# Performance work log

Measured on AMD Instinct MI355X. Metric: run time of the kernel, lower is better.

Reference implementation:

```python
import jax, jax.numpy as jnp
import numpy as np

D = 1024
B = 16
SP = 256
T = B * SP
DT_REF = 1.0
MAX_GROWTH = 0.3


def _cayley(re, im):
    A = re + 1j * im
    A = A - A.conj().T  # skew-Hermitian part
    I = jnp.eye(A.shape[0], dtype=A.dtype)
    return jnp.linalg.solve(I + A, I - A)


def _dft_basis(d):
    n = jnp.arange(d)
    k = jnp.arange(d)[:, None]
    ang = -2.0 * jnp.pi * (k * n).astype(jnp.float32) / d
    return jnp.exp(1j * ang) / jnp.sqrt(jnp.float32(d))


def _forward(x_input, h_prev_re, h_prev_im, xg_re, xg_im, flux_re, flux_im, dt,
             u_raw_re, u_raw_im, v_raw_re, v_raw_im, log_sigma, dft_weight,
             decay_re, decay_im, Wi, bi, Wo, bo, Wg, bg,
             ld, lf, law_re, law_im, base_noise, Wu1, bu1, Wu2, bu2,
             noise_re, noise_im):
    d = x_input.shape[-1]
    # ---- basis.encode ----
    V = _cayley(v_raw_re, v_raw_im)                       # [D,D] complex
    s_diag = jnp.exp(log_sigma).astype(V.dtype)
    xc = x_input.astype(jnp.complex64)
    alpha = jax.nn.sigmoid(dft_weight)
    x_tilde = (xc @ V) * s_diag * (1.0 - alpha) + (xc @ _dft_basis(d)) * alpha
    x_tilde = x_tilde[:, None, :]                          # [T,1,D]
    # ---- flux_tracker.forward_step ----
    fdecay = jax.nn.sigmoid(decay_re) + 1j * decay_im
    x_cat = jnp.concatenate([xg_re, xg_im], axis=-1)       # [B,2D]
    xin = x_cat @ Wi.T + bi
    update = xin[..., :d] + 1j * xin[..., d:]
    flux_next = (flux_re + 1j * flux_im) * fdecay + update
    s_cat = jnp.concatenate([flux_next.real, flux_next.imag], axis=-1)
    proj = s_cat @ Wo.T + bo
    source = proj[..., :d] + 1j * proj[..., d:]            # [B,D] complex
    gate = jax.nn.sigmoid(s_cat @ Wg.T + bg)               # [B,D] real
    # ---- transition operators ----
    l_re = jnp.tanh(-jnp.exp(ld) + law_re) * MAX_GROWTH
    lam = l_re + 1j * (lf + law_im)
    dt_ratio = dt / DT_REF                                 # [1]
    op_decay = jnp.exp(lam[None, :] * dt_ratio[:, None].astype(jnp.complex64))
    op_forcing = (op_decay - 1.0) / (lam[None, :] + 1e-8)
    # ---- expand source/gate over spatial ----
    bsz = source.shape[0]
    sp = x_tilde.shape[0] // bsz
    src = jnp.broadcast_to(source[:, None, None, :], (bsz, sp, 1, d)).reshape(-1, 1, d)
    g = jnp.broadcast_to(gate[:, None, None, :], (bsz, sp, 1, d)).reshape(-1, 1, d)
    forcing = x_tilde * g + src * (1.0 - g)
    h_prev = h_prev_re + 1j * h_prev_im
    h_next = h_prev * op_decay + forcing * op_forcing      # [T,1,D]
    # ---- SDE stochastic term ----
    base_var = base_noise ** 2 * jnp.expm1(2.0 * l_re * dt_ratio[:, None]) / (2.0 * l_re + 1e-8)
    base_var = jnp.maximum(base_var, 0.0)                  # [1,D]
    h_mean = h_next.mean(axis=1).real                      # [T,D]
    u = jax.nn.softplus(jax.nn.silu(h_mean @ Wu1.T + bu1) @ Wu2.T + bu2)  # [T,D]
    std = jnp.sqrt(base_var * u)[:, None, :].astype(h_next.dtype)          # [T,1,D]
    noise = (noise_re + 1j * noise_im) * jnp.sqrt(jnp.float32(0.5))
    return h_next + noise * std, flux_next


def setup_inputs() -> dict:
    key = jax.random.key(0)
    ks = jax.random.split(key, 40)
    rn = lambda i, shp, sc=1.0: jax.random.normal(ks[i], shp, jnp.float32) * sc
    q_re = jnp.linalg.qr(rn(0, (D, D)))[0]
    q_im = jnp.linalg.qr(rn(1, (D, D)))[0]
    return {
        "x_input": rn(2, (T, D)),
        "h_prev_re": rn(3, (T, 1, D)), "h_prev_im": rn(4, (T, 1, D)),
        "xg_re": rn(5, (B, D)), "xg_im": rn(6, (B, D)),
        "flux_re": rn(7, (B, D)), "flux_im": rn(8, (B, D)),
        "dt": jnp.ones((1,), jnp.float32),
        "u_raw_re": q_re * 0.1, "u_raw_im": q_im * 0.1,
        "v_raw_re": q_re.T * 0.1, "v_raw_im": q_im.T * 0.1,
        "log_sigma": jnp.zeros((D,), jnp.float32),
        "dft_weight": jnp.float32(0.2),
        "decay_re": rn(9, (D,), 0.1) - 1.0, "decay_im": rn(10, (D,), 0.1),
        "Wi": rn(11, (2 * D, 2 * D), 0.02), "bi": jnp.zeros((2 * D,), jnp.float32),
        "Wo": rn(12, (2 * D, 2 * D), 0.02), "bo": jnp.zeros((2 * D,), jnp.float32),
        "Wg": rn(13, (D, 2 * D), 0.02), "bg": jnp.zeros((D,), jnp.float32),
        "ld": rn(14, (D,), 0.5) - 2.0, "lf": rn(15, (D,), 1.0),
        "law_re": rn(16, (D,), 0.01), "law_im": rn(17, (D,), 0.01),
        "base_noise": jnp.float32(0.01),
        "Wu1": rn(18, (D // 4, D), 0.03), "bu1": jnp.zeros((D // 4,), jnp.float32),
        "Wu2": rn(19, (D, D // 4), 0.06), "bu2": jnp.zeros((D,), jnp.float32),
        "noise_re": rn(20, (T, 1, D)), "noise_im": rn(21, (T, 1, D)),
    }


def reference(x_input, h_prev_re, h_prev_im, xg_re, xg_im, flux_re, flux_im, dt,
              u_raw_re, u_raw_im, v_raw_re, v_raw_im, log_sigma, dft_weight,
              decay_re, decay_im, Wi, bi, Wo, bo, Wg, bg,
              ld, lf, law_re, law_im, base_noise, Wu1, bu1, Wu2, bu2,
              noise_re, noise_im):
    return _forward(x_input, h_prev_re, h_prev_im, xg_re, xg_im, flux_re, flux_im, dt,
                    u_raw_re, u_raw_im, v_raw_re, v_raw_im, log_sigma, dft_weight,
                    decay_re, decay_im, Wi, bi, Wo, bo, Wg, bg,
                    ld, lf, law_re, law_im, base_noise, Wu1, bu1, Wu2, bu2,
                    noise_re, noise_im)
```

## Files before the change

### kernel.cpp

```cpp
#include <hip/hip_runtime.h>
#include <cstddef>

#define TPB 256
#define TPB2 512

typedef short bf8v  __attribute__((ext_vector_type(8)));
typedef float f32x4 __attribute__((ext_vector_type(4)));
typedef unsigned short u16;

#define PSZ 2048
#define PSZ2 4096
#define LSTR 40
#define BUF1 2560
#define CSTR 68

static __device__ __forceinline__ u16 f2bf(float x) {
  unsigned int u = __float_as_uint(x);
  u = (u + 0x7FFFu + ((u >> 16) & 1u)) >> 16;
  return (u16)u;
}
static __device__ __forceinline__ float bf2f(u16 x) {
  return __uint_as_float(((unsigned int)x) << 16);
}
static __device__ __forceinline__ float sigmoidf_(float x) {
  return 1.0f / (1.0f + __expf(-x));
}
static __device__ __forceinline__ float spf_(float v) {
  return (v > 15.0f) ? v : __logf(1.0f + __expf(v));
}
static __device__ __forceinline__ bf8v neg8(bf8v a) {
  #pragma unroll
  for (int i = 0; i < 8; ++i) a[i] ^= (short)0x8000;
  return a;
}
static __device__ __forceinline__ void pack8(const float4& x, const float4& y,
                                             u16* dst) {
  unsigned int* d = (unsigned int*)dst;
  d[0] = ((unsigned)f2bf(x.y) << 16) | f2bf(x.x);
  d[1] = ((unsigned)f2bf(x.w) << 16) | f2bf(x.z);
  d[2] = ((unsigned)f2bf(y.y) << 16) | f2bf(y.x);
  d[3] = ((unsigned)f2bf(y.w) << 16) | f2bf(y.z);
}
static __device__ __forceinline__ uint2 packbf4(float a, float b, float c, float d) {
  uint2 r;
  r.x = ((unsigned)f2bf(b) << 16) | f2bf(a);
  r.y = ((unsigned)f2bf(d) << 16) | f2bf(c);
  return r;
}
static __device__ __forceinline__ void gload16(const u16* g, u16* l) {
  __builtin_amdgcn_global_load_lds((const __attribute__((address_space(1))) void*)g,
                                   (__attribute__((address_space(3))) void*)l,
                                   16, 0, 0);
}
static __device__ __forceinline__ bf8v fragld(const u16* plane, int r, int kq) {
  int kb = (kq << 4) ^ (((r >> 1) & 3) << 4);
  return *(const bf8v*)(plane + r * 32 + (kb >> 1));
}
static __device__ __forceinline__ bf8v fragld2(const u16* plane, int r, int kq, int s) {
  int ch = ((s << 2) + kq) ^ (r & 7);
  return *(const bf8v*)(plane + r * 64 + (ch << 3));
}
static __device__ __forceinline__ int swz8(int flat, int T) {
  return (flat & 7) * (T >> 3) + (flat >> 3);
}

#define WAITV(n) asm volatile("s_waitcnt vmcnt(" #n ")" ::: "memory")

__global__ __launch_bounds__(TPB) void build_a_k(
    const float* __restrict__ vre, const float* __restrict__ vim,
    u16* __restrict__ Ar, u16* __restrict__ Ai,
    u16* __restrict__ Nr, u16* __restrict__ Ni)
{
  int idx = blockIdx.x * TPB + threadIdx.x;
  int i = idx >> 10, j = idx & 1023;
  float ar = vre[idx] - vre[j * 1024 + i];
  float ai = vim[idx] + vim[j * 1024 + i];
  float dg = (i == j) ? 1.0f : 0.0f;
  Ar[idx] = f2bf(ar);       Ai[idx] = f2bf(ai);
  Nr[idx] = f2bf(dg - ar);  Ni[idx] = f2bf(-ai);
}

#define CG_VARS                                                              \
  int lane = tid & 63;                                                       \
  int wr = (tid >> 7) & 1, wc = (tid >> 6) & 1;                              \
  int lr8_ = ((tid & 63) >> 3) + ((tid >> 6) << 4);                          \
  int ks2_ = (((lane & 7) ^ (lane >> 3)) << 3);                              \
  u16* Lw_ = lds + ((tid >> 6) << 10);                                       \
  f32x4 accR[2][2] = {};                                                     \
  f32x4 accI[2][2] = {};

#define CG_STAGE(buf, k0, PAr, PAi, PBr, PBi)                                \
  { u16* Lb = Lw_ + (buf) * (4 * PSZ2);                                      \
    gload16((PAr) + (size_t)(bm + lr8_) * 1024 + (k0) + ks2_,     Lb + 0 * PSZ2);       \
    gload16((PAr) + (size_t)(bm + lr8_ + 8) * 1024 + (k0) + ks2_, Lb + 0 * PSZ2 + 512); \
    gload16((PAi) + (size_t)(bm + lr8_) * 1024 + (k0) + ks2_,     Lb + 1 * PSZ2);       \
    gload16((PAi) + (size_t)(bm + lr8_ + 8) * 1024 + (k0) + ks2_, Lb + 1 * PSZ2 + 512); \
    gload16((PBr) + (size_t)(bn + lr8_) * 1024 + (k0) + ks2_,     Lb + 2 * PSZ2);       \
    gload16((PBr) + (size_t)(bn + lr8_ + 8) * 1024 + (k0) + ks2_, Lb + 2 * PSZ2 + 512); \
    gload16((PBi) + (size_t)(bn + lr8_) * 1024 + (k0) + ks2_,     Lb + 3 * PSZ2);       \
    gload16((PBi) + (size_t)(bn + lr8_ + 8) * 1024 + (k0) + ks2_, Lb + 3 * PSZ2 + 512); }

#define CG_FRAGS(buf, s)                                                     \
  const u16* L = lds + (buf) * (4 * PSZ2);                                   \
  int rA = wr * 32 + (lane & 15);                                            \
  int rB = wc * 32 + (lane & 15);                                            \
  int kq = lane >> 4;                                                        \
  bf8v ar[2], ai[2], br[2], bi[2];                                           \
  ar[0] = fragld2(L + 0 * PSZ2, rA, kq, s);  ar[1] = fragld2(L + 0 * PSZ2, rA + 16, kq, s); \
  ai[0] = fragld2(L + 1 * PSZ2, rA, kq, s);  ai[1] = fragld2(L + 1 * PSZ2, rA + 16, kq, s); \
  br[0] = fragld2(L + 2 * PSZ2, rB, kq, s);  br[1] = fragld2(L + 2 * PSZ2, rB + 16, kq, s); \
  bi[0] = fragld2(L + 3 * PSZ2, rB, kq, s);  bi[1] = fragld2(L + 3 * PSZ2, rB + 16, kq, s);

#define CG_MFMA_BNEG0                                                        \
  { bf8v nbr[2] = { neg8(br[0]), neg8(br[1]) };                              \
    bf8v nbi[2] = { neg8(bi[0]), neg8(bi[1]) };                              \
    _Pragma("unroll")                                                        \
    for (int mf = 0; mf < 2; ++mf)                                           \
      _Pragma("unroll")                                                      \
      for (int nf = 0; nf < 2; ++nf) {                                       \
        accR[mf][nf] = __builtin_amdgcn_mfma_f32_16x16x32_bf16(ar[mf], nbr[nf], accR[mf][nf], 0, 0, 0); \
        accR[mf][nf] = __builtin_amdgcn_mfma_f32_16x16x32_bf16(ai[mf], nbi[nf], accR[mf][nf], 0, 0, 0); \
        accI[mf][nf] = __builtin_amdgcn_mfma_f32_16x16x32_bf16(ar[mf], bi[nf],  accI[mf][nf], 0, 0, 0); \
        accI[mf][nf] = __builtin_amdgcn_mfma_f32_16x16x32_bf16(ai[mf], nbr[nf], accI[mf][nf], 0, 0, 0); \
      } }

#define CG_MFMA_BNEG1                                                        \
  { bf8v nbi[2] = { neg8(bi[0]), neg8(bi[1]) };                              \
    _Pragma("unroll")                                                        \
    for (int mf = 0; mf < 2; ++mf)                                           \
      _Pragma("unroll")                                                      \
      for (int nf = 0; nf < 2; ++nf) {                                       \
        accR[mf][nf] = __builtin_amdgcn_mfma_f32_16x16x32_bf16(ar[mf], br[nf],  accR[mf][nf], 0, 0, 0); \
        accR[mf][nf] = __builtin_amdgcn_mfma_f32_16x16x32_bf16(ai[mf], bi[nf],  accR[mf][nf], 0, 0, 0); \
        accI[mf][nf] = __builtin_amdgcn_mfma_f32_16x16x32_bf16(ar[mf], nbi[nf], accI[mf][nf], 0, 0, 0); \
        accI[mf][nf] = __builtin_amdgcn_mfma_f32_16x16x32_bf16(ai[mf], br[nf],  accI[mf][nf], 0, 0, 0); \
      } }

#define CG_PIPELINE(MFMA_OP, PAr, PAi, PBr, PBi)                             \
  CG_STAGE(0, 0, PAr, PAi, PBr, PBi);                                        \
  _Pragma("unroll 1")                                                        \
  for (int t = 0; t < 16; ++t) {                                             \
    int bufc = t & 1;                                                        \
    if (t + 1 < 16) { CG_STAGE(bufc ^ 1, (t + 1) * 64, PAr, PAi, PBr, PBi);  \
                      WAITV(8); }                                            \
    else            { WAITV(0); }                                            \
    __builtin_amdgcn_sched_barrier(0);                                       \
    __builtin_amdgcn_s_barrier();                                            \
    __builtin_amdgcn_s_setprio(1);                                           \
    { CG_FRAGS(bufc, 0) MFMA_OP }                                            \
    { CG_FRAGS(bufc, 1) MFMA_OP }                                            \
    __builtin_amdgcn_s_setprio(0);                                           \
    __builtin_amdgcn_sched_barrier(0);                                       \
    __builtin_amdgcn_s_barrier();                                            \
  }

#define CG8_VARS                                                             \
  int lane = tid & 63;                                                       \
  int wv = tid >> 6;                                                         \
  int wq = wv & 3;                                                           \
  int wr = wq >> 1, wc = wq & 1;                                             \
  int sh = wv >> 2;                                                          \
  int ln8 = lane >> 3;                                                       \
  int ks2_ = (((lane & 7) ^ ln8) << 3);                                      \
  f32x4 accR[2][2] = {};                                                     \
  f32x4 accI[2][2] = {};

#define CG8_STAGE(buf, k0, PAr, PAi, PBr, PBi)                               \
  { u16* Lb = lds + (buf) * (4 * PSZ2);                                      \
    _Pragma("unroll")                                                        \
    for (int j = 0; j < 4; ++j) {                                            \
      int idx4 = wv * 4 + j;                                                 \
      int pl = idx4 >> 3, gr = idx4 & 7;                                     \
      const u16* src = (pl == 0) ? (PAr) : (pl == 1) ? (PAi)                 \
                      : (pl == 2) ? (PBr) : (PBi);                           \
      int base = (pl < 2) ? bm : bn;                                         \
      gload16(src + (size_t)(base + gr * 8 + ln8) * 1024 + (k0) + ks2_,      \
              Lb + pl * PSZ2 + gr * 512);                                    \
    } }

#define CG8_PIPELINE(MFMA_OP, PAr, PAi, PBr, PBi)                            \
  CG8_STAGE(0, 0, PAr, PAi, PBr, PBi);                                       \
  _Pragma("unroll 1")                                                        \
  for (int t = 0; t < 16; ++t) {                                             \
    int bufc = t & 1;                                                        \
    if (t + 1 < 16) { CG8_STAGE(bufc ^ 1, (t + 1) * 64, PAr, PAi, PBr, PBi); \
                      WAITV(4); }                                            \
    else            { WAITV(0); }                                            \
    __builtin_amdgcn_sched_barrier(0);                                       \
    __builtin_amdgcn_s_barrier();                                            \
    __builtin_amdgcn_s_setprio(1);                                           \
    { CG_FRAGS(bufc, sh) MFMA_OP }                                           \
    __builtin_amdgcn_s_setprio(0);                                           \
    __builtin_amdgcn_sched_barrier(0);                                       \
    __builtin_amdgcn_s_barrier();                                            \
  }

#define CG8_COMBINE                                                          \
  float* cmb = (float*)lds;                                                  \
  __syncthreads();                                                           \
  if (sh == 1) {                                                             \
    int cb = (wq * 64 + lane) * 33;                                          \
    _Pragma("unroll")                                                        \
    for (int mf = 0; mf < 2; ++mf)                                           \
      _Pragma("unroll")                                                      \
      for (int nf = 0; nf < 2; ++nf)                                         \
        _Pragma("unroll")                                                    \
        for (int r = 0; r < 4; ++r) {                                        \
          cmb[cb + (mf * 2 + nf) * 8 + r]     = accR[mf][nf][r];             \
          cmb[cb + (mf * 2 + nf) * 8 + 4 + r] = accI[mf][nf][r];             \
        }                                                                    \
  }                                                                          \
  __syncthreads();                                                           \
  if (sh == 0) {                                                             \
    int cb = (wq * 64 + lane) * 33;                                          \
    _Pragma("unroll")                                                        \
    for (int mf = 0; mf < 2; ++mf)                                           \
      _Pragma("unroll")                                                      \
      for (int nf = 0; nf < 2; ++nf)                                         \
        _Pragma("unroll")                                                    \
        for (int r = 0; r < 4; ++r) {                                        \
          accR[mf][nf][r] += cmb[cb + (mf * 2 + nf) * 8 + r];                \
          accI[mf][nf][r] += cmb[cb + (mf * 2 + nf) * 8 + 4 + r];            \
        }                                                                    \
  }

__global__ __launch_bounds__(TPB2) void d2_k(
    const u16* __restrict__ Apr, const u16* __restrict__ Api,
    u16* __restrict__ A2r, u16* __restrict__ A2i,
    const float* __restrict__ X, const float* __restrict__ Wu1,
    const float* __restrict__ Wu2,
    const float* __restrict__ ld, const float* __restrict__ lf,
    const float* __restrict__ law_re, const float* __restrict__ law_im,
    const float* __restrict__ dt, const float* __restrict__ base_noise,
    u16* __restrict__ Xb, u16* __restrict__ Wu1b, u16* __restrict__ Wu2b,
    float* __restrict__ od_re, float* __restrict__ od_im,
    float* __restrict__ of_re, float* __restrict__ of_im,
    float* __restrict__ bvar,
    const float* __restrict__ xg_re, const float* __restrict__ xg_im,
    const float* __restrict__ Wi, float* __restrict__ PpI)
{
  __shared__ __align__(16) u16 lds[2 * 4 * PSZ2];
  int tid = threadIdx.x;
  int bx = blockIdx.x;
  if (bx < 256) {
    int flat = swz8(bx, 256);
    int bm = (flat >> 4) * 64, bn = (flat & 15) * 64;
    CG8_VARS
    CG8_PIPELINE(CG_MFMA_BNEG0, Apr, Api, Apr, Api)
    CG8_COMBINE
    if (sh == 0) {
      #pragma unroll
      for (int mf = 0; mf < 2; ++mf)
        #pragma unroll
        for (int nf = 0; nf < 2; ++nf) {
          int col = bn + wc * 32 + nf * 16 + (lane & 15);
          #pragma unroll
          for (int r = 0; r < 4; ++r) {
            int rowg = bm + wr * 32 + mf * 16 + (lane >> 4) * 4 + r;
            size_t o = (size_t)rowg * 1024 + col;
            A2r[o] = f2bf(accR[mf][nf][r]);
            A2i[o] = f2bf(accI[mf][nf][r]);
          }
        }
    }
  } else if (bx < 1408) {
    int e = ((bx - 256) * TPB2 + tid) << 3;
    const float* src;
    u16* dst;
    if (e < 4194304)       { src = X + e;               dst = Xb + e; }
    else if (e < 4456448)  { src = Wu1 + (e - 4194304); dst = Wu1b + (e - 4194304); }
    else                   { src = Wu2 + (e - 4456448); dst = Wu2b + (e - 4456448); }
    float4 a = *(const float4*)src;
    float4 b = *(const float4*)(src + 4);
    u16 tmp[8];
    pack8(a, b, tmp);
    *(bf8v*)dst = *(bf8v*)tmp;
  } else if (bx < 1410) {
    int d = (bx - 1408) * TPB2 + tid;
    float dtr = dt[0];
    float lre = tanhf(-expf(ld[d]) + law_re[d]) * 0.3f;
    float lim = lf[d] + law_im[d];
    float er = expf(lre * dtr);
    float sn, cs;
    sincosf(lim * dtr, &sn, &cs);
    float odr = er * cs, odi = er * sn;
    od_re[d] = odr;  od_im[d] = odi;
    float numr = odr - 1.0f, numi = odi;
    float denr = lre + 1e-8f, deni = lim;
    float inv = 1.0f / (denr * denr + deni * deni);
    of_re[d] = (numr * denr + numi * deni) * inv;
    of_im[d] = (numi * denr - numr * deni) * inv;
    float bn2 = base_noise[0];
    float bv = bn2 * bn2 * expm1f(2.0f * lre * dtr) / (2.0f * lre + 1e-8f);
    bvar[d] = fmaxf(bv, 0.0f);
  } else {
    int id = bx - 1410;
    int c0 = (id & 31) * 64;
    int kbase = (id >> 5) * 256;
    bool act = tid < 256;
    int lane = tid & 63;
    int w = (tid >> 6) & 3;
    int row = (tid & 255) >> 2, kq = (tid & 3) << 3;

    f32x4 acc = {};
    float4 pb0, pb1;
    u16* sl = lds;

    auto gload = [&](int k0) {
      const float* p = Wi + (size_t)(c0 + row) * 2048 + k0 + kq;
      pb0 = *(const float4*)p; pb1 = *(const float4*)(p + 4);
    };
    auto stolds = [&](int buf) {
      pack8(pb0, pb1, sl + buf * BUF1 + row * LSTR + kq);
    };
    auto compute = [&](int buf, int k0) {
      int ar = lane & 15;
      int ko = (lane >> 4) * 8;
      const float* ap = (k0 < 1024) ? (xg_re + (size_t)ar * 1024 + k0 + ko)
                                    : (xg_im + (size_t)ar * 1024 + k0 + ko - 1024);
      float4 a0 = *(const float4*)ap, a1 = *(const float4*)(ap + 4);
      u16 abuf[8];
      pack8(a0, a1, abuf);
      bf8v af = *(bf8v*)abuf;
      bf8v bfr = *(const bf8v*)(sl + buf * BUF1 + (w * 16 + (lane & 15)) * LSTR + ko);
      acc = __builtin_amdgcn_mfma_f32_16x16x32_bf16(af, bfr, acc, 0, 0, 0);
    };

    if (act) { gload(kbase); stolds(0); }
    __syncthreads();
    int cur = 0;
    for (int t = 0; t < 8; ++t) {
      int k0 = kbase + t * 32;
      if (act) {
        if (t < 7) gload(k0 + 32);
        compute(cur, k0);
        if (t < 7) stolds(cur ^ 1);
      }
      __syncthreads();
      cur ^= 1;
    }
    if (act) {
      int c = c0 + w * 16 + (lane & 15);
      #pragma unroll
      for (int r = 0; r < 4; ++r) {
        int rr = (lane >> 4) * 4 + r;
        PpI[((size_t)(id >> 5) * 16 + rr) * 2048 + c] = acc[r];
      }
    }
  }
}

__global__ __launch_bounds__(TPB) void d3_k(
    const u16* __restrict__ A2r, const u16* __restrict__ A2i,
    const u16* __restrict__ Nr2, const u16* __restrict__ Ni2,
    u16* __restrict__ A4r, u16* __restrict__ A4i,
    u16* __restrict__ T1r, u16* __restrict__ T1i,
    const float* __restrict__ PpI, const float* __restrict__ bi,
    float* __restrict__ xin)
{
  __shared__ __align__(16) u16 lds[2 * 4 * PSZ2];
  int tid = threadIdx.x;
  int bx = blockIdx.x;
  if (bx < 512) {
    int flat = swz8(bx, 512);
    int z = flat >> 8;
    int t8 = flat & 255;
    int bm = (t8 >> 4) * 64, bn = (t8 & 15) * 64;
    const u16* Apr = z ? Nr2 : A2r;
    const u16* Api = z ? Ni2 : A2i;
    u16* Cr16 = z ? T1r : A4r;
    u16* Ci16 = z ? T1i : A4i;
    CG_VARS
    CG_PIPELINE(CG_MFMA_BNEG1, Apr, Api, A2r, A2i)
    #pragma unroll
    for (int mf = 0; mf < 2; ++mf)
      #pragma unroll
      for (int nf = 0; nf < 2; ++nf) {
        int col = bn + wc * 32 + nf * 16 + (lane & 15);
        #pragma unroll
        for (int r = 0; r < 4; ++r) {
          int rowg = bm + wr * 32 + mf * 16 + (lane >> 4) * 4 + r;
          size_t o = (size_t)rowg * 1024 + col;
          float vr = accR[mf][nf][r], vi = accI[mf][nf][r];
          if (z) { vr += bf2f(Nr2[o]); vi += bf2f(Ni2[o]); }
          Cr16[o] = f2bf(vr);
          Ci16[o] = f2bf(vi);
        }
      }
  } else {
    int idx = (bx - 512) * TPB + tid;
    int c = idx & 2047;
    float v = bi[c];
    #pragma unroll
    for (int s = 0; s < 8; ++s) v += PpI[(size_t)s * 32768 + idx];
    xin[idx] = v;
  }
}

__global__ __launch_bounds__(TPB2) void d4_k(
    const u16* __restrict__ T1r, const u16* __restrict__ T1i,
    const u16* __restrict__ A4r, const u16* __restrict__ A4i,
    const float* __restrict__ log_sigma, const float* __restrict__ dft_weight,
    u16* __restrict__ Mtr, u16* __restrict__ Mti,
    const float* __restrict__ xin,
    const float* __restrict__ flux_re, const float* __restrict__ flux_im,
    const float* __restrict__ decay_re, const float* __restrict__ decay_im,
    float* __restrict__ FNr, float* __restrict__ FNi,
    float* __restrict__ out1)
{
  __shared__ __align__(16) u16 lds[2 * 4 * PSZ2];
  int tid = threadIdx.x;
  int bx = blockIdx.x;
  if (bx < 256) {
    int flat = swz8(bx, 256);
    int bm = (flat >> 4) * 64, bn = (flat & 15) * 64;
    CG8_VARS
    CG8_PIPELINE(CG_MFMA_BNEG1, T1r, T1i, A4r, A4i)
    CG8_COMBINE

    u16* mtLr = lds;
    u16* mtLi = lds + 4608;
    __syncthreads();
    if (sh == 0) {
      float alpha = sigmoidf_(dft_weight[0]);
      const float isq = 0.03125f * alpha;
      #pragma unroll
      for (int mf = 0; mf < 2; ++mf)
        #pragma unroll
        for (int nf = 0; nf < 2; ++nf) {
          int dl = wc * 32 + nf * 16 + (lane & 15);
          int dgl = bn + dl;
          float w1 = expf(log_sigma[dgl]) * (1.0f - alpha);
          #pragma unroll
          for (int r = 0; r < 4; ++r) {
            int kl = wr * 32 + mf * 16 + (lane >> 4) * 4 + r;
            int kgl = bm + kl;
            size_t o = (size_t)kgl * 1024 + dgl;
            float dg = (kgl == dgl) ? 1.0f : 0.0f;
            float vr = 2.0f * accR[mf][nf][r] + 2.0f * bf2f(T1r[o]) - dg;
            float vi = 2.0f * accI[mf][nf][r] + 2.0f * bf2f(T1i[o]);
            int mm = (kgl * dgl) & 1023;
            float ang = -6.283185307179586f * (float)mm * (1.0f / 1024.0f);
            float sn, cs;
            sincosf(ang, &sn, &cs);
            mtLr[dl * 72 + kl] = f2bf(vr * w1 + cs * isq);
            mtLi[dl * 72 + kl] = f2bf(vi * w1 + sn * isq);
          }
        }
    }
    __syncthreads();
    if (tid < 256) {
      int dl = tid >> 2, kl0 = (tid & 3) * 16;
      size_t o = (size_t)(bn + dl) * 1024 + bm + kl0;
      uint4* srcR = (uint4*)(mtLr + dl * 72 + kl0);
      uint4* srcI = (uint4*)(mtLi + dl * 72 + kl0);
      *(uint4*)(Mtr + o)     = srcR[0];
      *(uint4*)(Mtr + o + 8) = srcR[1];
      *(uint4*)(Mti + o)     = srcI[0];
      *(uint4*)(Mti + o + 8) = srcI[1];
    }
  } else {
    int idx = (bx - 256) * TPB2 + tid;
    int b = idx >> 10, d = idx & 1023;
    float fdr = sigmoidf_(decay_re[d]);
    float fdi = decay_im[d];
    float fr = flux_re[idx], fi = flux_im[idx];
    float ur = xin[b * 2048 + d], ui = xin[b * 2048 + 1024 + d];
    float nr = fr * fdr - fi * fdi + ur;
    float ni = fr * fdi + fi * fdr + ui;
    FNr[idx] = nr;  FNi[idx] = ni;
    out1[idx] = nr;
  }
}

__global__ __launch_bounds__(TPB) void sgemm16_wog_k(
    const float* __restrict__ A0, const float* __restrict__ A1,
    const float* __restrict__ Wo, const float* __restrict__ Wg,
    float* __restrict__ PpO, float* __restrict__ PpG)
{
  __shared__ __align__(16) u16 lds[2 * BUF1];
  int tid = threadIdx.x;
  int bx = blockIdx.x;
  const float* Bw = (bx < 32) ? Wo : Wg;
  float* Pp = (bx < 32) ? PpO : PpG;
  int N = (bx < 32) ? 2048 : 1024;
  int c0 = ((bx < 32) ? bx : (bx - 32)) * 64;
  int kbase = blockIdx.y * 256;
  int lane = tid & 63;
  int w = tid >> 6;
  int row = tid >> 2, kq = (tid & 3) << 3;

  f32x4 acc = {};
  float4 pb0, pb1;

  auto gload = [&](int k0) {
    const float* p = Bw + (size_t)(c0 + row) * 2048 + k0 + kq;
    pb0 = *(const float4*)p; pb1 = *(const float4*)(p + 4);
  };
  auto stolds = [&](int buf) {
    pack8(pb0, pb1, lds + buf * BUF1 + row * LSTR + kq);
  };
  auto compute = [&](int buf, int k0) {
    int ar = lane & 15;
    int ko = (lane >> 4) * 8;
    const float* ap = (k0 < 1024) ? (A0 + (size_t)ar * 1024 + k0 + ko)
                                  : (A1 + (size_t)ar * 1024 + k0 + ko - 1024);
    float4 a0 = *(const float4*)ap, a1 = *(const float4*)(ap + 4);
    u16 abuf[8];
    pack8(a0, a1, abuf);
    bf8v af = *(bf8v*)abuf;
    const u16* L = lds + buf * BUF1;
    bf8v bfr = *(const bf8v*)(L + (w * 16 + (lane & 15)) * LSTR + ko);
    acc = __builtin_amdgcn_mfma_f32_16x16x32_bf16(af, bfr, acc, 0, 0, 0);
  };

  gload(kbase); stolds(0); __syncthreads();
  int cur = 0;
  for (int t = 0; t < 8; ++t) {
    int k0 = kbase + t * 32;
    if (t < 7) gload(k0 + 32);
    compute(cur, k0);
    if (t < 7) stolds(cur ^ 1);
    __syncthreads();
    cur ^= 1;
  }

  int c = c0 + w * 16 + (lane & 15);
  #pragma unroll
  for (int r = 0; r < 4; ++r) {
    int rr = (lane >> 4) * 4 + r;
    Pp[((size_t)blockIdx.y * 16 + rr) * N + c] = acc[r];
  }
}

__global__ __launch_bounds__(TPB) void red16_wog_k(
    const float* __restrict__ PpO, const float* __restrict__ PpG,
    const float* __restrict__ bo, const float* __restrict__ bg,
    float* __restrict__ proj, float* __restrict__ gate)
{
  int idx = blockIdx.x * TPB + threadIdx.x;
  if (idx < 32768) {
    int c = idx & 2047;
    float v = bo[c];
    #pragma unroll
    for (int s = 0; s < 8; ++s) v += PpO[(size_t)s * 32768 + idx];
    proj[idx] = v;
  } else {
    int j = idx - 32768;
    int c = j & 1023;
    float v = bg[c];
    #pragma unroll
    for (int s = 0; s < 8; ++s) v += PpG[(size_t)s * 16384 + j];
    gate[j] = sigmoidf_(v);
  }
}

__global__ __launch_bounds__(TPB) void xmh_nt_k(
    const u16* __restrict__ Xb,
    const u16* __restrict__ Mtr, const u16* __restrict__ Mti,
    const float* __restrict__ gate, const float* __restrict__ proj,
    const float* __restrict__ od_re, const float* __restrict__ od_im,
    const float* __restrict__ of_re, const float* __restrict__ of_im,
    const float* __restrict__ hp_re, const float* __restrict__ hp_im,
    u16* __restrict__ Hrb)
{
  __shared__ __align__(16) u16 lds[2 * 16384];
  int flat = swz8(blockIdx.x, 512);
  int bm = (flat >> 4) * 128, bn = (flat & 15) * 64;
  int tid = threadIdx.x;
  int lane = tid & 63;
  int w = tid >> 6;
  int wr = w >> 1, wc = w & 1;
  int ln8 = lane >> 3;
  int ks2_ = (((lane & 7) ^ ln8) << 3);

  f32x4 accR[4][2] = {};
  f32x4 accI[4][2] = {};

#define XM_STAGE(buf, k0)                                                    \
  { u16* Lb = lds + (buf) * 16384;                                           \
    _Pragma("unroll")                                                        \
    for (int g = 0; g < 4; ++g)                                              \
      gload16(Xb + (size_t)(bm + w * 32 + g * 8 + ln8) * 1024 + (k0) + ks2_, \
              Lb + (w * 32 + g * 8) * 64);                                   \
    _Pragma("unroll")                                                        \
    for (int g = 0; g < 2; ++g) {                                            \
      gload16(Mtr + (size_t)(bn + w * 16 + g * 8 + ln8) * 1024 + (k0) + ks2_,\
              Lb + 8192 + (w * 16 + g * 8) * 64);                            \
      gload16(Mti + (size_t)(bn + w * 16 + g * 8 + ln8) * 1024 + (k0) + ks2_,\
              Lb + 12288 + (w * 16 + g * 8) * 64);                           \
    } }
#define XM_COMPUTE(buf, s)                                                   \
  { const u16* L = lds + (buf) * 16384;                                      \
    int kq = lane >> 4;                                                      \
    bf8v a[4], br[2], bi[2];                                                 \
    _Pragma("unroll")                                                        \
    for (int mf = 0; mf < 4; ++mf)                                           \
      a[mf] = fragld2(L, wr * 64 + mf * 16 + (lane & 15), kq, s);            \
    _Pragma("unroll")                                                        \
    for (int nf = 0; nf < 2; ++nf) {                                         \
      br[nf] = fragld2(L + 8192,  wc * 32 + nf * 16 + (lane & 15), kq, s);   \
      bi[nf] = fragld2(L + 12288, wc * 32 + nf * 16 + (lane & 15), kq, s);   \
    }                                                                        \
    _Pragma("unroll")                                                        \
    for (int mf = 0; mf < 4; ++mf)                                           \
      _Pragma("unroll")                                                      \
      for (int nf = 0; nf < 2; ++nf) {                                       \
        accR[mf][nf] = __builtin_amdgcn_mfma_f32_16x16x32_bf16(a[mf], br[nf], accR[mf][nf], 0, 0, 0); \
        accI[mf][nf] = __builtin_amdgcn_mfma_f32_16x16x32_bf16(a[mf], bi[nf], accI[mf][nf], 0, 0, 0); \
      } }

  XM_STAGE(0, 0);
  #pragma unroll 1
  for (int t = 0; t < 16; ++t) {
    int bufc = t & 1;
    if (t + 1 < 16) { XM_STAGE(bufc ^ 1, (t + 1) * 64); WAITV(8); }
    else            { WAITV(0); }
    __builtin_amdgcn_sched_barrier(0);
    __builtin_amdgcn_s_barrier();
    __builtin_amdgcn_s_setprio(1);
    XM_COMPUTE(bufc, 0)
    XM_COMPUTE(bufc, 1)
    __builtin_amdgcn_s_setprio(0);
    __builtin_amdgcn_sched_barrier(0);
    __builtin_amdgcn_s_barrier();
  }

  #pragma unroll
  for (int mf = 0; mf < 4; ++mf)
    #pragma unroll
    for (int nf = 0; nf < 2; ++nf) {
      int c = bn + wc * 32 + nf * 16 + (lane & 15);
      #pragma unroll
      for (int r = 0; r < 4; ++r) {
        int t = bm + wr * 64 + mf * 16 + (lane >> 4) * 4 + r;
        int b = t >> 8;
        float g  = gate[b * 1024 + c];
        float sr = proj[b * 2048 + c];
        float si = proj[b * 2048 + 1024 + c];
        float fr = accR[mf][nf][r] * g + sr * (1.0f - g);
        float fi = accI[mf][nf][r] * g + si * (1.0f - g);
        float odr = od_re[c], odi = od_im[c];
        float ofr = of_re[c], ofi = of_im[c];
        size_t off = (size_t)t * 1024 + c;
        float pr = hp_re[off], pi = hp_im[off];
        Hrb[off] = f2bf(pr * odr - pi * odi + fr * ofr - fi * ofi);
      }
    }
}

template<int KI, int EPI>
__global__ __launch_bounds__(TPB) void rgemm_nt_k(
    const u16* __restrict__ A, const u16* __restrict__ B,
    const float* __restrict__ bias,
    u16* __restrict__ C16, int nbxl, int total)
{
  __shared__ __align__(16) u16 lds[3 * 2 * PSZ];
  const int K = KI * 32;
  int tid = threadIdx.x;
  int flat = swz8(blockIdx.x, total);
  int bm = (flat >> nbxl) * 64;
  int bn = (flat & ((1 << nbxl) - 1)) * 64;
  const int N = 64 << nbxl;
  int lane = tid & 63;
  int wr = (tid >> 7) & 1, wc = (tid >> 6) & 1;
  int lr_ = ((tid & 63) >> 2) + ((tid >> 6) << 4);
  int ks_ = (((tid & 3) ^ ((tid >> 3) & 3)) << 3);
  u16* Lw_ = lds + ((tid >> 6) << 9);

  f32x4 acc[2][2] = {};

#define RG_STAGE(buf, k0)                                                    \
  { u16* Lb = Lw_ + (buf) * (2 * PSZ);                                       \
    gload16(A + (size_t)(bm + lr_) * K + (k0) + ks_, Lb + 0 * PSZ);          \
    gload16(B + (size_t)(bn + lr_) * K + (k0) + ks_, Lb + 1 * PSZ); }
#define RG_COMPUTE(buf)                                                      \
  { const u16* L = lds + (buf) * (2 * PSZ);                                  \
    int rA = wr * 32 + (lane & 15);                                          \
    int rB = wc * 32 + (lane & 15);                                          \
    int kq = lane >> 4;                                                      \
    bf8v a[2], b[2];                                                         \
    a[0] = fragld(L + 0 * PSZ, rA, kq);  a[1] = fragld(L + 0 * PSZ, rA + 16, kq); \
    b[0] = fragld(L + 1 * PSZ, rB, kq);  b[1] = fragld(L + 1 * PSZ, rB + 16, kq); \
    _Pragma("unroll")                                                        \
    for (int mf = 0; mf < 2; ++mf)                                           \
      _Pragma("unroll")                                                      \
      for (int nf = 0; nf < 2; ++nf)                                         \
        acc[mf][nf] = __builtin_amdgcn_mfma_f32_16x16x32_bf16(a[mf], b[nf], acc[mf][nf], 0, 0, 0); }

  RG_STAGE(0, 0);
  RG_STAGE(1, 32);
  #pragma unroll 1
  for (int t = 0; t < KI; ++t) {
    int bufc = t % 3;
    if (t + 2 < KI) { RG_STAGE((t + 2) % 3, (t + 2) * 32); }
    if (t + 2 < KI)      { WAITV(4); }
    else if (t + 1 < KI) { WAITV(2); }
    else                 { WAITV(0); }
    __builtin_amdgcn_sched_barrier(0);
    __builtin_amdgcn_s_barrier();
    __builtin_amdgcn_s_setprio(1);
    RG_COMPUTE(bufc)
    __builtin_amdgcn_s_setprio(0);
    __builtin_amdgcn_sched_barrier(0);
    __builtin_amdgcn_s_barrier();
  }

  if constexpr (EPI == 0) {
    #pragma unroll
    for (int mf = 0; mf < 2; ++mf)
      #pragma unroll
      for (int nf = 0; nf < 2; ++nf) {
        int c = bn + wc * 32 + nf * 16 + (lane & 15);
        #pragma unroll
        for (int r = 0; r < 4; ++r) {
          int t = bm + wr * 32 + mf * 16 + (lane >> 4) * 4 + r;
          float v = acc[mf][nf][r] + bias[c];
          v = v * sigmoidf_(v);
          C16[(size_t)t * N + c] = f2bf(v);
        }
      }
  } else {
    float* ct = (float*)lds;
    __syncthreads();
    #pragma unroll
    for (int mf = 0; mf < 2; ++mf)
      #pragma unroll
      for (int nf = 0; nf < 2; ++nf) {
        int rbase = wr * 32 + mf * 16 + (lane >> 4) * 4;
        int cc = wc * 32 + nf * 16 + (lane & 15);
        #pragma unroll
        for (int r = 0; r < 4; ++r)
          ct[(rbase + r) * CSTR + cc] = acc[mf][nf][r];
      }
    __syncthreads();
    int w = tid >> 6, l = tid & 63;
    int lcol = (l & 15) * 4;
    #pragma unroll
    for (int p = 0; p < 4; ++p) {
      int lrow = w * 16 + p * 4 + (l >> 4);
      int t = bm + lrow;
      int c = bn + lcol;
      float4 v4 = *(float4*)&ct[lrow * CSTR + lcol];
      float4 bi4 = *(const float4*)(bias + c);
      float u0 = spf_(v4.x + bi4.x);
      float u1 = spf_(v4.y + bi4.y);
      float u2 = spf_(v4.z + bi4.z);
      float u3 = spf_(v4.w + bi4.w);
      *(uint2*)(C16 + (size_t)t * N + c) = packbf4(u0, u1, u2, u3);
    }
  }
}

__global__ __launch_bounds__(TPB) void fin_k(
    const u16* __restrict__ Hrb, const u16* __restrict__ ub,
    const float* __restrict__ nre, const float* __restrict__ bvar,
    float* __restrict__ out0)
{
  int idx = (blockIdx.x * TPB + threadIdx.x) << 3;
  int c = idx & 1023;
  bf8v hb = *(const bf8v*)(Hrb + idx);
  bf8v uv = *(const bf8v*)(ub + idx);
  float4 n0 = *(const float4*)(nre + idx);
  float4 n1 = *(const float4*)(nre + idx + 4);
  float4 b0 = *(const float4*)(bvar + c);
  float4 b1 = *(const float4*)(bvar + c + 4);
  float4 o0, o1;
  const float s2 = 0.7071067811865476f;
  #pragma unroll
  for (int j = 0; j < 4; ++j) {
    float sc = sqrtf(((const float*)&b0)[j] * bf2f((u16)uv[j])) * s2;
    ((float*)&o0)[j] = bf2f((u16)hb[j]) + ((const float*)&n0)[j] * sc;
  }
  #pragma unroll
  for (int j = 0; j < 4; ++j) {
    float sc = sqrtf(((const float*)&b1)[j] * bf2f((u16)uv[4 + j])) * s2;
    ((float*)&o1)[j] = bf2f((u16)hb[4 + j]) + ((const float*)&n1)[j] * sc;
  }
  *(float4*)(out0 + idx)     = o0;
  *(float4*)(out0 + idx + 4) = o1;
}

extern "C" void kernel_launch(void* const* d_in, const int* in_sizes, int n_in,
                              void* d_out, int out_size, void* d_ws, size_t ws_size,
                              hipStream_t stream) {
  (void)in_sizes; (void)n_in; (void)out_size;

  const float* x_input    = (const float*)d_in[0];
  const float* h_prev_re  = (const float*)d_in[1];
  const float* h_prev_im  = (const float*)d_in[2];
  const float* xg_re      = (const float*)d_in[3];
  const float* xg_im      = (const float*)d_in[4];
  const float* flux_re    = (const float*)d_in[5];
  const float* flux_im    = (const float*)d_in[6];
  const float* dt         = (const float*)d_in[7];
  const float* v_raw_re   = (const float*)d_in[10];
  const float* v_raw_im   = (const float*)d_in[11];
  const float* log_sigma  = (const float*)d_in[12];
  const float* dft_weight = (const float*)d_in[13];
  const float* decay_re   = (const float*)d_in[14];
  const float* decay_im   = (const float*)d_in[15];
  const float* Wi_in      = (const float*)d_in[16];
  const float* bi         = (const float*)d_in[17];
  const float* Wo         = (const float*)d_in[18];
  const float* bo         = (const float*)d_in[19];
  const float* Wg         = (const float*)d_in[20];
  const float* bg         = (const float*)d_in[21];
  const float* ld         = (const float*)d_in[22];
  const float* lf         = (const float*)d_in[23];
  const float* law_re     = (const float*)d_in[24];
  const float* law_im     = (const float*)d_in[25];
  const float* base_noise = (const float*)d_in[26];
  const float* Wu1        = (const float*)d_in[27];
  const float* bu1        = (const float*)d_in[28];
  const float* Wu2        = (const float*)d_in[29];
  const float* bu2        = (const float*)d_in[30];
  const float* noise_re   = (const float*)d_in[31];

  const size_t PL16 = 1024ull * 1024ull;
  if (ws_size < 16 * PL16 * 2) return;

  u16* P = (u16*)d_ws;
  u16* Ar  = P + 0 * PL16;   u16* Ai  = P + 1 * PL16;
  u16* Nr  = P + 2 * PL16;   u16* Ni  = P + 3 * PL16;
  u16* A2r = P + 4 * PL16;   u16* A2i = P + 5 * PL16;
  u16* A4r = P + 6 * PL16;   u16* A4i = P + 7 * PL16;
  u16* T1r = P + 8 * PL16;   u16* T1i = P + 9 * PL16;
  u16* Mtr = P + 2 * PL16;   u16* Mti = P + 3 * PL16;
  u16* Xb  = P + 10 * PL16;
  u16* Hrb = P + 4 * PL16;
  u16* ub  = P + 0 * PL16;
  float* PpO = (float*)(P + 0 * PL16);
  float* PpG = PpO + 262144;
  float* PpI = (float*)(P + 14 * PL16);
  u16* mlp1b = P + 14 * PL16;
  u16* Wu1b  = P + 15 * PL16;
  u16* Wu2b  = Wu1b + 262144;
  float* sm  = (float*)(P + 15 * PL16 + 524288);
  float* xin  = sm;
  float* proj = xin + 32768;
  float* FNr  = proj + 32768;
  float* FNi  = FNr + 16384;
  float* gate = FNi + 16384;
  float* od_re = gate + 16384;
  float* od_im = od_re + 1024;
  float* of_re = od_im + 1024;
  float* of_im = of_re + 1024;
  float* bvar  = of_im + 1024;

  float* out0f = (float*)d_out;
  float* out1f = out0f + (size_t)4096 * 1024;

  build_a_k<<<4096, TPB, 0, stream>>>(v_raw_re, v_raw_im, Ar, Ai, Nr, Ni);
  d2_k<<<1666, TPB2, 0, stream>>>(Ar, Ai, A2r, A2i,
                                  x_input, Wu1, Wu2,
                                  ld, lf, law_re, law_im, dt, base_noise,
                                  Xb, Wu1b, Wu2b,
                                  od_re, od_im, of_re, of_im, bvar,
                                  xg_re, xg_im, Wi_in, PpI);
  d3_k<<<640, TPB, 0, stream>>>(A2r, A2i, Nr, Ni, A4r, A4i, T1r, T1i,
                                PpI, bi, xin);
  d4_k<<<288, TPB2, 0, stream>>>(T1r, T1i, A4r, A4i, log_sigma, dft_weight,
                                 Mtr, Mti,
                                 xin, flux_re, flux_im, decay_re, decay_im,
                                 FNr, FNi, out1f);
  sgemm16_wog_k<<<dim3(48, 8), TPB, 0, stream>>>(FNr, FNi, Wo, Wg, PpO, PpG);
  red16_wog_k<<<192, TPB, 0, stream>>>(PpO, PpG, bo, bg, proj, gate);
  xmh_nt_k<<<512, TPB, 0, stream>>>(Xb, Mtr, Mti, gate, proj,
                                    od_re, od_im, of_re, of_im,
                                    h_prev_re, h_prev_im, Hrb);
  rgemm_nt_k<32, 0><<<256, TPB, 0, stream>>>(Hrb, Wu1b, bu1, mlp1b, 2, 256);
  rgemm_nt_k<8, 2><<<1024, TPB, 0, stream>>>(mlp1b, Wu2b, bu2, ub, 4, 1024);
  fin_k<<<2048, TPB, 0, stream>>>(Hrb, ub, noise_re, bvar, out0f);
}
```

Before: 136.4 us.

## Replace split-K 512-thread complex GEMM tiles with 64x32 tiles at 256 threads

The d2 and d4 complex bf16 GEMMs move from 64x64 output tiles, where eight waves split K in half and combine partial sums through LDS, to 64x32 tiles with four waves each covering the full K range. This doubles the block count to 512 and removes the LDS combine step and its extra barriers. The side tasks fused into d2 and d4 (bf16 conversion, operator precompute, small GEMV, flux update) are reindexed for 256-thread blocks. The cost is that A tiles are now loaded by twice as many blocks, raising global and L2 traffic, and each wave does less MFMA work per LDS fragment load.

```diff
diff --git a/kernel.cpp b/kernel.cpp
--- a/kernel.cpp
+++ b/kernel.cpp
@@ -2,7 +2,6 @@
 #include <cstddef>
 
 #define TPB 256
-#define TPB2 512
 
 typedef short bf8v  __attribute__((ext_vector_type(8)));
 typedef float f32x4 __attribute__((ext_vector_type(4)));
@@ -13,6 +12,7 @@
 #define LSTR 40
 #define BUF1 2560
 #define CSTR 68
+#define RTBUF 12288
 
 static __device__ __forceinline__ u16 f2bf(float x) {
   unsigned int u = __float_as_uint(x);
@@ -110,19 +110,6 @@
   ai[0] = fragld2(L + 1 * PSZ2, rA, kq, s);  ai[1] = fragld2(L + 1 * PSZ2, rA + 16, kq, s); \
   br[0] = fragld2(L + 2 * PSZ2, rB, kq, s);  br[1] = fragld2(L + 2 * PSZ2, rB + 16, kq, s); \
   bi[0] = fragld2(L + 3 * PSZ2, rB, kq, s);  bi[1] = fragld2(L + 3 * PSZ2, rB + 16, kq, s);
-
-#define CG_MFMA_BNEG0                                                        \
-  { bf8v nbr[2] = { neg8(br[0]), neg8(br[1]) };                              \
-    bf8v nbi[2] = { neg8(bi[0]), neg8(bi[1]) };                              \
-    _Pragma("unroll")                                                        \
-    for (int mf = 0; mf < 2; ++mf)                                           \
-      _Pragma("unroll")                                                      \
-      for (int nf = 0; nf < 2; ++nf) {                                       \
-        accR[mf][nf] = __builtin_amdgcn_mfma_f32_16x16x32_bf16(ar[mf], nbr[nf], accR[mf][nf], 0, 0, 0); \
-        accR[mf][nf] = __builtin_amdgcn_mfma_f32_16x16x32_bf16(ai[mf], nbi[nf], accR[mf][nf], 0, 0, 0); \
-        accI[mf][nf] = __builtin_amdgcn_mfma_f32_16x16x32_bf16(ar[mf], bi[nf],  accI[mf][nf], 0, 0, 0); \
-        accI[mf][nf] = __builtin_amdgcn_mfma_f32_16x16x32_bf16(ai[mf], nbr[nf], accI[mf][nf], 0, 0, 0); \
-      } }
 
 #define CG_MFMA_BNEG1                                                        \
   { bf8v nbi[2] = { neg8(bi[0]), neg8(bi[1]) };                              \
@@ -154,77 +141,87 @@
     __builtin_amdgcn_s_barrier();                                            \
   }
 
-#define CG8_VARS                                                             \
+#define CGRT_VARS                                                            \
   int lane = tid & 63;                                                       \
   int wv = tid >> 6;                                                         \
-  int wq = wv & 3;                                                           \
-  int wr = wq >> 1, wc = wq & 1;                                             \
-  int sh = wv >> 2;                                                          \
+  int wr = wv >> 1, wc = wv & 1;                                             \
   int ln8 = lane >> 3;                                                       \
   int ks2_ = (((lane & 7) ^ ln8) << 3);                                      \
-  f32x4 accR[2][2] = {};                                                     \
-  f32x4 accI[2][2] = {};
-
-#define CG8_STAGE(buf, k0, PAr, PAi, PBr, PBi)                               \
-  { u16* Lb = lds + (buf) * (4 * PSZ2);                                      \
-    _Pragma("unroll")                                                        \
-    for (int j = 0; j < 4; ++j) {                                            \
-      int idx4 = wv * 4 + j;                                                 \
-      int pl = idx4 >> 3, gr = idx4 & 7;                                     \
-      const u16* src = (pl == 0) ? (PAr) : (pl == 1) ? (PAi)                 \
-                      : (pl == 2) ? (PBr) : (PBi);                           \
-      int base = (pl < 2) ? bm : bn;                                         \
-      gload16(src + (size_t)(base + gr * 8 + ln8) * 1024 + (k0) + ks2_,      \
-              Lb + pl * PSZ2 + gr * 512);                                    \
+  f32x4 accR[2] = {};                                                        \
+  f32x4 accI[2] = {};
+
+#define CGRT_STAGE(buf, k0, PAr, PAi, PBr, PBi)                              \
+  { u16* Lb = lds + (buf) * RTBUF;                                           \
+    _Pragma("unroll")                                                        \
+    for (int j = 0; j < 6; ++j) {                                            \
+      int idx = wv * 6 + j;                                                  \
+      const u16* src; int row; int doff;                                     \
+      if (idx < 16) {                                                        \
+        int pl = idx >> 3, gr = idx & 7;                                     \
+        src = pl ? (PAi) : (PAr);                                            \
+        row = bm + gr * 8 + ln8;                                             \
+        doff = pl * 4096 + gr * 512;                                         \
+      } else {                                                               \
+        int i2 = idx - 16;                                                   \
+        int pl = i2 >> 2, gr = i2 & 3;                                       \
+        src = pl ? (PBi) : (PBr);                                            \
+        row = bn + gr * 8 + ln8;                                             \
+        doff = 8192 + pl * 2048 + gr * 512;                                  \
+      }                                                                      \
+      gload16(src + (size_t)row * 1024 + (k0) + ks2_, Lb + doff);            \
     } }
 
-#define CG8_PIPELINE(MFMA_OP, PAr, PAi, PBr, PBi)                            \
-  CG8_STAGE(0, 0, PAr, PAi, PBr, PBi);                                       \
+#define CGRT_FRAGS(buf, s)                                                   \
+  const u16* L = lds + (buf) * RTBUF;                                        \
+  int rA = wr * 32 + (lane & 15);                                            \
+  int rB = wc * 16 + (lane & 15);                                            \
+  int kq = lane >> 4;                                                        \
+  bf8v ar[2], ai[2], br1, bi1;                                               \
+  ar[0] = fragld2(L, rA, kq, s);          ar[1] = fragld2(L, rA + 16, kq, s);          \
+  ai[0] = fragld2(L + 4096, rA, kq, s);   ai[1] = fragld2(L + 4096, rA + 16, kq, s);   \
+  br1 = fragld2(L + 8192, rB, kq, s);                                        \
+  bi1 = fragld2(L + 10240, rB, kq, s);
+
+#define CGRT_MFMA_BNEG0                                                      \
+  { bf8v nbr = neg8(br1);                                                    \
+    bf8v nbi = neg8(bi1);                                                    \
+    _Pragma("unroll")                                                        \
+    for (int mf = 0; mf < 2; ++mf) {                                         \
+      accR[mf] = __builtin_amdgcn_mfma_f32_16x16x32_bf16(ar[mf], nbr, accR[mf], 0, 0, 0); \
+      accR[mf] = __builtin_amdgcn_mfma_f32_16x16x32_bf16(ai[mf], nbi, accR[mf], 0, 0, 0); \
+      accI[mf] = __builtin_amdgcn_mfma_f32_16x16x32_bf16(ar[mf], bi1, accI[mf], 0, 0, 0); \
+      accI[mf] = __builtin_amdgcn_mfma_f32_16x16x32_bf16(ai[mf], nbr, accI[mf], 0, 0, 0); \
+    } }
+
+#define CGRT_MFMA_BNEG1                                                      \
+  { bf8v nbi = neg8(bi1);                                                    \
+    _Pragma("unroll")                                                        \
+    for (int mf = 0; mf < 2; ++mf) {                                         \
+      accR[mf] = __builtin_amdgcn_mfma_f32_16x16x32_bf16(ar[mf], br1, accR[mf], 0, 0, 0); \
+      accR[mf] = __builtin_amdgcn_mfma_f32_16x16x32_bf16(ai[mf], bi1, accR[mf], 0, 0, 0); \
+      accI[mf] = __builtin_amdgcn_mfma_f32_16x16x32_bf16(ar[mf], nbi, accI[mf], 0, 0, 0); \
+      accI[mf] = __builtin_amdgcn_mfma_f32_16x16x32_bf16(ai[mf], br1, accI[mf], 0, 0, 0); \
+    } }
+
+#define CGRT_PIPELINE(MFMA_OP, PAr, PAi, PBr, PBi)                           \
+  CGRT_STAGE(0, 0, PAr, PAi, PBr, PBi);                                      \
   _Pragma("unroll 1")                                                        \
   for (int t = 0; t < 16; ++t) {                                             \
     int bufc = t & 1;                                                        \
-    if (t + 1 < 16) { CG8_STAGE(bufc ^ 1, (t + 1) * 64, PAr, PAi, PBr, PBi); \
-                      WAITV(4); }                                            \
+    if (t + 1 < 16) { CGRT_STAGE(bufc ^ 1, (t + 1) * 64, PAr, PAi, PBr, PBi);\
+                      WAITV(6); }                                            \
     else            { WAITV(0); }                                            \
     __builtin_amdgcn_sched_barrier(0);                                       \
     __builtin_amdgcn_s_barrier();                                            \
     __builtin_amdgcn_s_setprio(1);                                           \
-    { CG_FRAGS(bufc, sh) MFMA_OP }                                           \
+    { CGRT_FRAGS(bufc, 0) MFMA_OP }                                          \
+    { CGRT_FRAGS(bufc, 1) MFMA_OP }                                          \
     __builtin_amdgcn_s_setprio(0);                                           \
     __builtin_amdgcn_sched_barrier(0);                                       \
     __builtin_amdgcn_s_barrier();                                            \
   }
 
-#define CG8_COMBINE                                                          \
-  float* cmb = (float*)lds;                                                  \
-  __syncthreads();                                                           \
-  if (sh == 1) {                                                             \
-    int cb = (wq * 64 + lane) * 33;                                          \
-    _Pragma("unroll")                                                        \
-    for (int mf = 0; mf < 2; ++mf)                                           \
-      _Pragma("unroll")                                                      \
-      for (int nf = 0; nf < 2; ++nf)                                         \
-        _Pragma("unroll")                                                    \
-        for (int r = 0; r < 4; ++r) {                                        \
-          cmb[cb + (mf * 2 + nf) * 8 + r]     = accR[mf][nf][r];             \
-          cmb[cb + (mf * 2 + nf) * 8 + 4 + r] = accI[mf][nf][r];             \
-        }                                                                    \
-  }                                                                          \
-  __syncthreads();                                                           \
-  if (sh == 0) {                                                             \
-    int cb = (wq * 64 + lane) * 33;                                          \
-    _Pragma("unroll")                                                        \
-    for (int mf = 0; mf < 2; ++mf)                                           \
-      _Pragma("unroll")                                                      \
-      for (int nf = 0; nf < 2; ++nf)                                         \
-        _Pragma("unroll")                                                    \
-        for (int r = 0; r < 4; ++r) {                                        \
-          accR[mf][nf][r] += cmb[cb + (mf * 2 + nf) * 8 + r];                \
-          accI[mf][nf][r] += cmb[cb + (mf * 2 + nf) * 8 + 4 + r];            \
-        }                                                                    \
-  }
-
-__global__ __launch_bounds__(TPB2) void d2_k(
+__global__ __launch_bounds__(TPB) void d2_k(
     const u16* __restrict__ Apr, const u16* __restrict__ Api,
     u16* __restrict__ A2r, u16* __restrict__ A2i,
     const float* __restrict__ X, const float* __restrict__ Wu1,
@@ -239,32 +236,27 @@
     const float* __restrict__ xg_re, const float* __restrict__ xg_im,
     const float* __restrict__ Wi, float* __restrict__ PpI)
 {
-  __shared__ __align__(16) u16 lds[2 * 4 * PSZ2];
+  __shared__ __align__(16) u16 lds[2 * RTBUF];
   int tid = threadIdx.x;
   int bx = blockIdx.x;
-  if (bx < 256) {
-    int flat = swz8(bx, 256);
-    int bm = (flat >> 4) * 64, bn = (flat & 15) * 64;
-    CG8_VARS
-    CG8_PIPELINE(CG_MFMA_BNEG0, Apr, Api, Apr, Api)
-    CG8_COMBINE
-    if (sh == 0) {
+  if (bx < 512) {
+    int flat = swz8(bx, 512);
+    int bm = (flat >> 5) * 64, bn = (flat & 31) * 32;
+    CGRT_VARS
+    CGRT_PIPELINE(CGRT_MFMA_BNEG0, Apr, Api, Apr, Api)
+    #pragma unroll
+    for (int mf = 0; mf < 2; ++mf) {
+      int col = bn + wc * 16 + (lane & 15);
       #pragma unroll
-      for (int mf = 0; mf < 2; ++mf)
-        #pragma unroll
-        for (int nf = 0; nf < 2; ++nf) {
-          int col = bn + wc * 32 + nf * 16 + (lane & 15);
-          #pragma unroll
-          for (int r = 0; r < 4; ++r) {
-            int rowg = bm + wr * 32 + mf * 16 + (lane >> 4) * 4 + r;
-            size_t o = (size_t)rowg * 1024 + col;
-            A2r[o] = f2bf(accR[mf][nf][r]);
-            A2i[o] = f2bf(accI[mf][nf][r]);
-          }
-        }
+      for (int r = 0; r < 4; ++r) {
+        int rowg = bm + wr * 32 + mf * 16 + (lane >> 4) * 4 + r;
+        size_t o = (size_t)rowg * 1024 + col;
+        A2r[o] = f2bf(accR[mf][r]);
+        A2i[o] = f2bf(accI[mf][r]);
+      }
     }
-  } else if (bx < 1408) {
-    int e = ((bx - 256) * TPB2 + tid) << 3;
+  } else if (bx < 2816) {
+    int e = ((bx - 512) * TPB + tid) << 3;
     const float* src;
     u16* dst;
     if (e < 4194304)       { src = X + e;               dst = Xb + e; }
@@ -275,8 +267,8 @@
     u16 tmp[8];
     pack8(a, b, tmp);
     *(bf8v*)dst = *(bf8v*)tmp;
-  } else if (bx < 1410) {
-    int d = (bx - 1408) * TPB2 + tid;
+  } else if (bx < 2820) {
+    int d = (bx - 2816) * TPB + tid;
     float dtr = dt[0];
     float lre = tanhf(-expf(ld[d]) + law_re[d]) * 0.3f;
     float lim = lf[d] + law_im[d];
@@ -294,13 +286,12 @@
     float bv = bn2 * bn2 * expm1f(2.0f * lre * dtr) / (2.0f * lre + 1e-8f);
     bvar[d] = fmaxf(bv, 0.0f);
   } else {
-    int id = bx - 1410;
+    int id = bx - 2820;
     int c0 = (id & 31) * 64;
     int kbase = (id >> 5) * 256;
-    bool act = tid < 256;
     int lane = tid & 63;
-    int w = (tid >> 6) & 3;
-    int row = (tid & 255) >> 2, kq = (tid & 3) << 3;
+    int w = tid >> 6;
+    int row = tid >> 2, kq = (tid & 3) << 3;
 
     f32x4 acc = {};
     float4 pb0, pb1;
@@ -326,26 +317,21 @@
       acc = __builtin_amdgcn_mfma_f32_16x16x32_bf16(af, bfr, acc, 0, 0, 0);
     };
 
-    if (act) { gload(kbase); stolds(0); }
-    __syncthreads();
+    gload(kbase); stolds(0); __syncthreads();
     int cur = 0;
     for (int t = 0; t < 8; ++t) {
       int k0 = kbase + t * 32;
-      if (act) {
-        if (t < 7) gload(k0 + 32);
-        compute(cur, k0);
-        if (t < 7) stolds(cur ^ 1);
-      }
+      if (t < 7) gload(k0 + 32);
+      compute(cur, k0);
+      if (t < 7) stolds(cur ^ 1);
       __syncthreads();
       cur ^= 1;
     }
-    if (act) {
-      int c = c0 + w * 16 + (lane & 15);
-      #pragma unroll
-      for (int r = 0; r < 4; ++r) {
-        int rr = (lane >> 4) * 4 + r;
-        PpI[((size_t)(id >> 5) * 16 + rr) * 2048 + c] = acc[r];
-      }
+    int c = c0 + w * 16 + (lane & 15);
+    #pragma unroll
+    for (int r = 0; r < 4; ++r) {
+      int rr = (lane >> 4) * 4 + r;
+      PpI[((size_t)(id >> 5) * 16 + rr) * 2048 + c] = acc[r];
     }
   }
 }
@@ -397,7 +383,7 @@
   }
 }
 
-__global__ __launch_bounds__(TPB2) void d4_k(
+__global__ __launch_bounds__(TPB) void d4_k(
     const u16* __restrict__ T1r, const u16* __restrict__ T1i,
     const u16* __restrict__ A4r, const u16* __restrict__ A4i,
     const float* __restrict__ log_sigma, const float* __restrict__ dft_weight,
@@ -408,59 +394,52 @@
     float* __restrict__ FNr, float* __restrict__ FNi,
     float* __restrict__ out1)
 {
-  __shared__ __align__(16) u16 lds[2 * 4 * PSZ2];
+  __shared__ __align__(16) u16 lds[2 * RTBUF];
   int tid = threadIdx.x;
   int bx = blockIdx.x;
-  if (bx < 256) {
-    int flat = swz8(bx, 256);
-    int bm = (flat >> 4) * 64, bn = (flat & 15) * 64;
-    CG8_VARS
-    CG8_PIPELINE(CG_MFMA_BNEG1, T1r, T1i, A4r, A4i)
-    CG8_COMBINE
+  if (bx < 512) {
+    int flat = swz8(bx, 512);
+    int bm = (flat >> 5) * 64, bn = (flat & 31) * 32;
+    CGRT_VARS
+    CGRT_PIPELINE(CGRT_MFMA_BNEG1, T1r, T1i, A4r, A4i)
 
     u16* mtLr = lds;
-    u16* mtLi = lds + 4608;
+    u16* mtLi = lds + 2304;
     __syncthreads();
-    if (sh == 0) {
+    {
       float alpha = sigmoidf_(dft_weight[0]);
       const float isq = 0.03125f * alpha;
       #pragma unroll
-      for (int mf = 0; mf < 2; ++mf)
+      for (int mf = 0; mf < 2; ++mf) {
+        int dl = wc * 16 + (lane & 15);
+        int dgl = bn + dl;
+        float w1 = expf(log_sigma[dgl]) * (1.0f - alpha);
         #pragma unroll
-        for (int nf = 0; nf < 2; ++nf) {
-          int dl = wc * 32 + nf * 16 + (lane & 15);
-          int dgl = bn + dl;
-          float w1 = expf(log_sigma[dgl]) * (1.0f - alpha);
-          #pragma unroll
-          for (int r = 0; r < 4; ++r) {
-            int kl = wr * 32 + mf * 16 + (lane >> 4) * 4 + r;
-            int kgl = bm + kl;
-            size_t o = (size_t)kgl * 1024 + dgl;
-            float dg = (kgl == dgl) ? 1.0f : 0.0f;
-            float vr = 2.0f * accR[mf][nf][r] + 2.0f * bf2f(T1r[o]) - dg;
-            float vi = 2.0f * accI[mf][nf][r] + 2.0f * bf2f(T1i[o]);
-            int mm = (kgl * dgl) & 1023;
-            float ang = -6.283185307179586f * (float)mm * (1.0f / 1024.0f);
-            float sn, cs;
-            sincosf(ang, &sn, &cs);
-            mtLr[dl * 72 + kl] = f2bf(vr * w1 + cs * isq);
-            mtLi[dl * 72 + kl] = f2bf(vi * w1 + sn * isq);
-          }
+        for (int r = 0; r < 4; ++r) {
+          int kl = wr * 32 + mf * 16 + (lane >> 4) * 4 + r;
+          int kgl = bm + kl;
+          size_t o = (size_t)kgl * 1024 + dgl;
+          float dg = (kgl == dgl) ? 1.0f : 0.0f;
+          float vr = 2.0f * accR[mf][r] + 2.0f * bf2f(T1r[o]) - dg;
+          float vi = 2.0f * accI[mf][r] + 2.0f * bf2f(T1i[o]);
+          int mm = (kgl * dgl) & 1023;
+          float ang = -6.283185307179586f * (float)mm * (1.0f / 1024.0f);
+          float sn, cs;
+          sincosf(ang, &sn, &cs);
+          mtLr[dl * 72 + kl] = f2bf(vr * w1 + cs * isq);
+          mtLi[dl * 72 + kl] = f2bf(vi * w1 + sn * isq);
         }
+      }
     }
     __syncthreads();
-    if (tid < 256) {
-      int dl = tid >> 2, kl0 = (tid & 3) * 16;
+    {
+      int dl = tid >> 3, kl0 = (tid & 7) * 8;
       size_t o = (size_t)(bn + dl) * 1024 + bm + kl0;
-      uint4* srcR = (uint4*)(mtLr + dl * 72 + kl0);
-      uint4* srcI = (uint4*)(mtLi + dl * 72 + kl0);
-      *(uint4*)(Mtr + o)     = srcR[0];
-      *(uint4*)(Mtr + o + 8) = srcR[1];
-      *(uint4*)(Mti + o)     = srcI[0];
-      *(uint4*)(Mti + o + 8) = srcI[1];
+      *(uint4*)(Mtr + o) = *(uint4*)(mtLr + dl * 72 + kl0);
+      *(uint4*)(Mti + o) = *(uint4*)(mtLi + dl * 72 + kl0);
     }
   } else {
-    int idx = (bx - 256) * TPB2 + tid;
+    int idx = (bx - 512) * TPB + tid;
     int b = idx >> 10, d = idx & 1023;
     float fdr = sigmoidf_(decay_re[d]);
     float fdi = decay_im[d];
@@ -852,18 +831,18 @@
   float* out1f = out0f + (size_t)4096 * 1024;
 
   build_a_k<<<4096, TPB, 0, stream>>>(v_raw_re, v_raw_im, Ar, Ai, Nr, Ni);
-  d2_k<<<1666, TPB2, 0, stream>>>(Ar, Ai, A2r, A2i,
-                                  x_input, Wu1, Wu2,
-                                  ld, lf, law_re, law_im, dt, base_noise,
-                                  Xb, Wu1b, Wu2b,
-                                  od_re, od_im, of_re, of_im, bvar,
-                                  xg_re, xg_im, Wi_in, PpI);
+  d2_k<<<3076, TPB, 0, stream>>>(Ar, Ai, A2r, A2i,
+                                 x_input, Wu1, Wu2,
+                                 ld, lf, law_re, law_im, dt, base_noise,
+                                 Xb, Wu1b, Wu2b,
+                                 od_re, od_im, of_re, of_im, bvar,
+                                 xg_re, xg_im, Wi_in, PpI);
   d3_k<<<640, TPB, 0, stream>>>(A2r, A2i, Nr, Ni, A4r, A4i, T1r, T1i,
                                 PpI, bi, xin);
-  d4_k<<<288, TPB2, 0, stream>>>(T1r, T1i, A4r, A4i, log_sigma, dft_weight,
-                                 Mtr, Mti,
-                                 xin, flux_re, flux_im, decay_re, decay_im,
-                                 FNr, FNi, out1f);
+  d4_k<<<576, TPB, 0, stream>>>(T1r, T1i, A4r, A4i, log_sigma, dft_weight,
+                                Mtr, Mti,
+                                xin, flux_re, flux_im, decay_re, decay_im,
+                                FNr, FNi, out1f);
   sgemm16_wog_k<<<dim3(48, 8), TPB, 0, stream>>>(FNr, FNi, Wo, Wg, PpO, PpG);
   red16_wog_k<<<192, TPB, 0, stream>>>(PpO, PpG, bo, bg, proj, gate);
   xmh_nt_k<<<512, TPB, 0, stream>>>(Xb, Mtr, Mti, gate, proj,
```

Result: no change. 134.7 us (-1.2%).
